# Performance work log

Hardware: AMD Instinct MI355X
Metric: run time of the kernel (lower is better)

The kernel has to match this reference:

```python
import jax, jax.numpy as jnp
import numpy as np
from jax import lax

B, L, W, C, H = 2, 64, 64, 128, 4
DH = C // H  # 32
SCALE = 32 ** -0.5  # dim_head ** -0.5
BN_EPS = 1e-3  # keras BatchNormalization default epsilon


def _sep_conv(x, dwk, dwb, g, b, mu, var, pwk, pwb):
    # Depthwise 3x3 conv, 'same' padding (NHWC, kernel HWIO with groups=C)
    y = lax.conv_general_dilated(
        x, dwk, window_strides=(1, 1), padding='SAME',
        dimension_numbers=('NHWC', 'HWIO', 'NHWC'),
        feature_group_count=x.shape[-1]) + dwb
    # BatchNorm (inference mode: moving statistics)
    y = g * (y - mu) * lax.rsqrt(var + BN_EPS) + b
    # Pointwise 1x1 conv
    return jnp.einsum('blwc,cf->blwf', y, pwk) + pwb


def setup_inputs() -> dict:
    key = jax.random.key(0)
    ks = jax.random.split(key, 32)
    d = {'x': jax.random.normal(ks[0], (B, L * W, C), dtype=jnp.float32)}
    i = 1
    for p in ('q', 'k', 'v'):
        d[p + '_dwk'] = jax.random.normal(ks[i], (3, 3, 1, C), jnp.float32) * 0.1; i += 1
        d[p + '_dwb'] = jax.random.normal(ks[i], (C,), jnp.float32) * 0.05; i += 1
        d[p + '_g'] = jnp.ones((C,), jnp.float32) + jax.random.normal(ks[i], (C,), jnp.float32) * 0.05; i += 1
        d[p + '_b'] = jax.random.normal(ks[i], (C,), jnp.float32) * 0.05; i += 1
        d[p + '_mu'] = jax.random.normal(ks[i], (C,), jnp.float32) * 0.05; i += 1
        d[p + '_var'] = jnp.abs(jax.random.normal(ks[i], (C,), jnp.float32) * 0.1) + 0.9; i += 1
        d[p + '_pwk'] = jax.random.normal(ks[i], (C, C), jnp.float32) * (C ** -0.5); i += 1
        d[p + '_pwb'] = jax.random.normal(ks[i], (C,), jnp.float32) * 0.05; i += 1
    d['out_w'] = jax.random.normal(ks[i], (C, C), jnp.float32) * (C ** -0.5); i += 1
    d['out_b'] = jax.random.normal(ks[i], (C,), jnp.float32) * 0.05
    return d


def reference(x,
              q_dwk, q_dwb, q_g, q_b, q_mu, q_var, q_pwk, q_pwb,
              k_dwk, k_dwb, k_g, k_b, k_mu, k_var, k_pwk, k_pwb,
              v_dwk, v_dwb, v_g, v_b, v_mu, v_var, v_pwk, v_pwb,
              out_w, out_b):
    xi = x.reshape(B, L, W, C)  # 'b (l w) c -> b l w c'
    def heads(t):  # 'b l w (h d) -> b h (l w) d'
        return t.reshape(B, L * W, H, DH).transpose(0, 2, 1, 3)
    q = heads(_sep_conv(xi, q_dwk, q_dwb, q_g, q_b, q_mu, q_var, q_pwk, q_pwb))
    k = heads(_sep_conv(xi, k_dwk, k_dwb, k_g, k_b, k_mu, k_var, k_pwk, k_pwb))
    v = heads(_sep_conv(xi, v_dwk, v_dwb, v_g, v_b, v_mu, v_var, v_pwk, v_pwb))
    dots = jnp.einsum('bhid,bhjd->bhij', q, k) * SCALE
    attn = jax.nn.softmax(dots, axis=-1)
    out = jnp.einsum('bhij,bhjd->bhid', attn, v)
    out = out.transpose(0, 2, 1, 3).reshape(B, L * W, C)  # 'b h c d -> b c (h d)'
    return out @ out_w + out_b  # to_out Dense (dropout is identity at inference)
```

## Files before the change

### kernel.cpp

```cpp
#include <hip/hip_runtime.h>
#include <hip/hip_bf16.h>

#define NN 4096
#define CC 128

typedef __bf16 bf16x8_t __attribute__((ext_vector_type(8)));
typedef __bf16 bf16x4_t __attribute__((ext_vector_type(4)));
typedef float f32x4 __attribute__((ext_vector_type(4)));

static constexpr float SCALE = 0.17677669529663687f;
static constexpr float BN_EPS = 1e-3f;

struct PrecompArgs {
    const float *g[3], *b[3], *mu[3], *var[3], *dwb[3], *pwk[3], *pwb[3];
    float *Wp[3], *bias[3];
};

__global__ void precomp_kernel(PrecompArgs A) {
    int q = blockIdx.x;
    int f = threadIdx.x;
    const float* pwk = A.pwk[q];
    float* Wp = A.Wp[q];
    float bias = A.pwb[q][f];
    for (int c = 0; c < 128; ++c) {
        float rs = rsqrtf(A.var[q][c] + BN_EPS);
        float s = A.g[q][c] * rs;
        float w = pwk[c * 128 + f];
        Wp[c * 128 + f] = s * w;
        bias += (s * (A.dwb[q][c] - A.mu[q][c]) + A.b[q][c]) * w;
    }
    A.bias[q][f] = bias;
}

struct ConvArgs {
    const float* x;
    const float* dwk[3];
    const float* Wp[3];
    const float* bias[3];
    __bf16* out[3];
};

__global__ __launch_bounds__(256) void conv_kernel(ConvArgs A) {
    int qkv  = blockIdx.x >> 8;
    int tile = blockIdx.x & 255;
    int b    = tile >> 7;
    int t32  = tile & 127;
    int n0   = t32 * 32;
    int l    = n0 >> 6;
    int w0   = n0 & 63;
    int tid  = threadIdx.x;

    __shared__ float dwl[32][128];

    const float* dwk = A.dwk[qkv];
    {
        int c  = tid & 127;
        int ph = tid >> 7;
        float kd[9];
#pragma unroll
        for (int t = 0; t < 9; ++t) kd[t] = dwk[t * 128 + c];
        float acc[16];
#pragma unroll
        for (int j = 0; j < 16; ++j) acc[j] = 0.f;
        int wbase = w0 + ph * 16;
        const float* xb = A.x + (size_t)b * NN * CC + c;
#pragma unroll
        for (int dl = 0; dl < 3; ++dl) {
            int ll = l + dl - 1;
            if (ll < 0 || ll >= 64) continue;
#pragma unroll
            for (int wx = 0; wx < 18; ++wx) {
                int ww = wbase + wx - 1;
                if (ww < 0 || ww >= 64) continue;
                float xv = xb[(ll * 64 + ww) * 128];
                if (wx < 16)               acc[wx]     += xv * kd[dl * 3 + 0];
                if (wx >= 1 && wx < 17)    acc[wx - 1] += xv * kd[dl * 3 + 1];
                if (wx >= 2)               acc[wx - 2] += xv * kd[dl * 3 + 2];
            }
        }
#pragma unroll
        for (int j = 0; j < 16; ++j) dwl[ph * 16 + j][c] = acc[j];
    }
    __syncthreads();
    {
        int fg = tid & 31;
        int pg = tid >> 5;
        const float* Wp = A.Wp[qkv];
        float a[4][4];
#pragma unroll
        for (int i = 0; i < 4; ++i)
#pragma unroll
            for (int j = 0; j < 4; ++j) a[i][j] = 0.f;
        for (int c = 0; c < 128; ++c) {
            f32x4 wv = *(const f32x4*)&Wp[c * 128 + fg * 4];
#pragma unroll
            for (int i = 0; i < 4; ++i) {
                float d = dwl[pg * 4 + i][c];
                a[i][0] += d * wv[0];
                a[i][1] += d * wv[1];
                a[i][2] += d * wv[2];
                a[i][3] += d * wv[3];
            }
        }
        f32x4 bs = *(const f32x4*)&A.bias[qkv][fg * 4];
        int f0 = fg * 4;
        int h  = f0 >> 5;
        int dh0 = f0 & 31;
        __bf16* dst = A.out[qkv] + ((size_t)(b * 4 + h) * NN) * 32 + dh0;
#pragma unroll
        for (int i = 0; i < 4; ++i) {
            int n = n0 + pg * 4 + i;
            bf16x4_t v;
            v[0] = (__bf16)(a[i][0] + bs[0]);
            v[1] = (__bf16)(a[i][1] + bs[1]);
            v[2] = (__bf16)(a[i][2] + bs[2]);
            v[3] = (__bf16)(a[i][3] + bs[3]);
            *(bf16x4_t*)(dst + (size_t)n * 32) = v;
        }
    }
}

__global__ __launch_bounds__(512, 1) void attn_kernel(
        const __bf16* __restrict__ qg, const __bf16* __restrict__ kg,
        const __bf16* __restrict__ vg, float* __restrict__ Og) {
    int bid = blockIdx.x;
    int bh  = bid >> 5;
    int qt  = bid & 31;
    int b   = bh >> 2, h = bh & 3;
    int tid = threadIdx.x;
    int wv  = tid >> 6;
    int lane = tid & 63;
    int lg  = lane >> 4;
    int lr  = lane & 15;

    __shared__ __bf16 Kl[64][40];
    __shared__ __bf16 Vt[32][88];
    __shared__ __bf16 Pl[8][16][88];

    const __bf16* qrow = qg + ((size_t)bh * NN + qt * 128 + wv * 16 + lr) * 32 + lg * 8;
    bf16x8_t Qf = *(const bf16x8_t*)qrow;
    const __bf16* Kbh = kg + (size_t)bh * NN * 32;
    const __bf16* Vbh = vg + (size_t)bh * NN * 32;

    f32x4 acc0 = {0.f, 0.f, 0.f, 0.f};
    f32x4 acc1 = {0.f, 0.f, 0.f, 0.f};
    f32x4 zero4 = {0.f, 0.f, 0.f, 0.f};
    float mr[4], ls[4];
#pragma unroll
    for (int r = 0; r < 4; ++r) { mr[r] = -1e30f; ls[r] = 0.f; }

    int srow = tid >> 3;
    int sc4  = (tid & 7) * 4;

    for (int t = 0; t < 64; ++t) {
        int k0 = t * 64;
        uint2 kkv = *(const uint2*)(Kbh + (size_t)(k0 + srow) * 32 + sc4);
        *(uint2*)&Kl[srow][sc4] = kkv;
        uint2 vvv = *(const uint2*)(Vbh + (size_t)(k0 + srow) * 32 + sc4);
        const __bf16* vp = (const __bf16*)&vvv;
#pragma unroll
        for (int j = 0; j < 4; ++j) Vt[sc4 + j][srow] = vp[j];
        __syncthreads();

        f32x4 s[4];
#pragma unroll
        for (int kb = 0; kb < 4; ++kb) {
            bf16x8_t Kf = *(const bf16x8_t*)&Kl[lr + kb * 16][lg * 8];
            s[kb] = __builtin_amdgcn_mfma_f32_16x16x32_bf16(Qf, Kf, zero4, 0, 0, 0);
        }
        float pr[4][4];
#pragma unroll
        for (int r = 0; r < 4; ++r) {
            float m = fmaxf(fmaxf(s[0][r], s[1][r]), fmaxf(s[2][r], s[3][r])) * SCALE;
            m = fmaxf(m, __shfl_xor(m, 1));
            m = fmaxf(m, __shfl_xor(m, 2));
            m = fmaxf(m, __shfl_xor(m, 4));
            m = fmaxf(m, __shfl_xor(m, 8));
            float mnew = fmaxf(mr[r], m);
            float alpha = __expf(mr[r] - mnew);
            mr[r] = mnew;
            float rsum = 0.f;
#pragma unroll
            for (int kb = 0; kb < 4; ++kb) {
                float p = __expf(s[kb][r] * SCALE - mnew);
                pr[kb][r] = p;
                rsum += p;
            }
            rsum += __shfl_xor(rsum, 1);
            rsum += __shfl_xor(rsum, 2);
            rsum += __shfl_xor(rsum, 4);
            rsum += __shfl_xor(rsum, 8);
            ls[r] = ls[r] * alpha + rsum;
            acc0[r] *= alpha;
            acc1[r] *= alpha;
        }
#pragma unroll
        for (int kb = 0; kb < 4; ++kb)
#pragma unroll
            for (int r = 0; r < 4; ++r)
                Pl[wv][lg * 4 + r][lr + kb * 16] = (__bf16)pr[kb][r];
        __syncthreads();
#pragma unroll
        for (int ks = 0; ks < 2; ++ks) {
            bf16x8_t Pf = *(const bf16x8_t*)&Pl[wv][lr][ks * 32 + lg * 8];
            bf16x8_t V0 = *(const bf16x8_t*)&Vt[lr][ks * 32 + lg * 8];
            bf16x8_t V1 = *(const bf16x8_t*)&Vt[lr + 16][ks * 32 + lg * 8];
            acc0 = __builtin_amdgcn_mfma_f32_16x16x32_bf16(Pf, V0, acc0, 0, 0, 0);
            acc1 = __builtin_amdgcn_mfma_f32_16x16x32_bf16(Pf, V1, acc1, 0, 0, 0);
        }
        __syncthreads();
    }
    int nrow = qt * 128 + wv * 16 + lg * 4;
    float* ob = Og + (size_t)b * NN * 128 + (size_t)h * 32;
#pragma unroll
    for (int r = 0; r < 4; ++r) {
        float inv = 1.f / ls[r];
        ob[(size_t)(nrow + r) * 128 + lr]      = acc0[r] * inv;
        ob[(size_t)(nrow + r) * 128 + lr + 16] = acc1[r] * inv;
    }
}

__global__ __launch_bounds__(256) void outproj_kernel(
        const float* __restrict__ Og, const float* __restrict__ ow,
        const float* __restrict__ obias, float* __restrict__ out) {
    int tile = blockIdx.x;
    int b = tile >> 7, t32 = tile & 127;
    int n0 = t32 * 32;
    int tid = threadIdx.x;
    __shared__ float Ol[32][128];
#pragma unroll
    for (int r2 = 0; r2 < 16; ++r2) {
        int idx = r2 * 256 + tid;
        int p = idx >> 7, c = idx & 127;
        Ol[p][c] = Og[((size_t)b * NN + n0 + p) * 128 + c];
    }
    __syncthreads();
    int fg = tid & 31, pg = tid >> 5;
    float a[4][4];
#pragma unroll
    for (int i = 0; i < 4; ++i)
#pragma unroll
        for (int j = 0; j < 4; ++j) a[i][j] = 0.f;
    for (int c = 0; c < 128; ++c) {
        f32x4 wv4 = *(const f32x4*)&ow[c * 128 + fg * 4];
#pragma unroll
        for (int i = 0; i < 4; ++i) {
            float d = Ol[pg * 4 + i][c];
            a[i][0] += d * wv4[0];
            a[i][1] += d * wv4[1];
            a[i][2] += d * wv4[2];
            a[i][3] += d * wv4[3];
        }
    }
    f32x4 bs = *(const f32x4*)&obias[fg * 4];
#pragma unroll
    for (int i = 0; i < 4; ++i) {
        int n = n0 + pg * 4 + i;
        f32x4 v;
        v[0] = a[i][0] + bs[0];
        v[1] = a[i][1] + bs[1];
        v[2] = a[i][2] + bs[2];
        v[3] = a[i][3] + bs[3];
        *(f32x4*)(out + ((size_t)b * NN + n) * 128 + fg * 4) = v;
    }
}

extern "C" void kernel_launch(void* const* d_in, const int* in_sizes, int n_in,
                              void* d_out, int out_size, void* d_ws, size_t ws_size,
                              hipStream_t stream) {
    const float* x = (const float*)d_in[0];
    char* ws = (char*)d_ws;

    float* Wp[3];
    float* biasp[3];
    __bf16* qkvp[3];
    for (int i = 0; i < 3; ++i) {
        Wp[i]    = (float*)(ws + (size_t)i * 65536);
        biasp[i] = (float*)(ws + 196608 + (size_t)i * 512);
        qkvp[i]  = (__bf16*)(ws + 262144 + (size_t)i * 2097152);
    }
    float* O = (float*)(ws + 262144 + 3 * (size_t)2097152);

    PrecompArgs pa;
    ConvArgs ca;
    ca.x = x;
    for (int i = 0; i < 3; ++i) {
        int base = 1 + 8 * i;
        ca.dwk[i] = (const float*)d_in[base + 0];
        pa.dwb[i] = (const float*)d_in[base + 1];
        pa.g[i]   = (const float*)d_in[base + 2];
        pa.b[i]   = (const float*)d_in[base + 3];
        pa.mu[i]  = (const float*)d_in[base + 4];
        pa.var[i] = (const float*)d_in[base + 5];
        pa.pwk[i] = (const float*)d_in[base + 6];
        pa.pwb[i] = (const float*)d_in[base + 7];
        pa.Wp[i] = Wp[i];
        pa.bias[i] = biasp[i];
        ca.Wp[i] = Wp[i];
        ca.bias[i] = biasp[i];
        ca.out[i] = qkvp[i];
    }

    hipLaunchKernelGGL(precomp_kernel, dim3(3), dim3(128), 0, stream, pa);
    hipLaunchKernelGGL(conv_kernel, dim3(768), dim3(256), 0, stream, ca);
    hipLaunchKernelGGL(attn_kernel, dim3(256), dim3(512), 0, stream,
                       qkvp[0], qkvp[1], qkvp[2], O);
    hipLaunchKernelGGL(outproj_kernel, dim3(256), dim3(256), 0, stream,
                       O, (const float*)d_in[25], (const float*)d_in[26],
                       (float*)d_out);
}
```

Measured before the change: 341.0 us.

## Restructure attention kernel: transposed S, register-resident P, double-buffered K/V, folded scale

Computes S transposed (K as the A operand) so each lane holds one query's 16 scores. P stays in registers as the MFMA A operand, which removes the P shared-memory round trip and one barrier per tile. K/V tiles are double-buffered with the next tile's global loads issued before compute, and the launch switches to 512 blocks of 256 threads with two blocks per CU. The softmax scale and log2e are folded into the Q projection weights in precomp so exp2f can be used without a per-element multiply. The cost is extra cross-lane shuffles to broadcast alpha and the row sum, plus more LDS for the double buffers.

```diff
diff --git a/kernel.cpp b/kernel.cpp
--- a/kernel.cpp
+++ b/kernel.cpp
@@ -9,6 +9,7 @@
 typedef float f32x4 __attribute__((ext_vector_type(4)));
 
 static constexpr float SCALE = 0.17677669529663687f;
+static constexpr float LOG2E = 1.4426950408889634f;
 static constexpr float BN_EPS = 1e-3f;
 
 struct PrecompArgs {
@@ -16,20 +17,28 @@
     float *Wp[3], *bias[3];
 };
 
-__global__ void precomp_kernel(PrecompArgs A) {
+__global__ __launch_bounds__(128) void precomp_kernel(PrecompArgs A) {
     int q = blockIdx.x;
     int f = threadIdx.x;
+    __shared__ float sS[128], sB[128];
+    {
+        int c = f;
+        float rs = rsqrtf(A.var[q][c] + BN_EPS);
+        float s = A.g[q][c] * rs;
+        sS[c] = s;
+        sB[c] = s * (A.dwb[q][c] - A.mu[q][c]) + A.b[q][c];
+    }
+    __syncthreads();
+    float qs = (q == 0) ? SCALE * LOG2E : 1.0f;
     const float* pwk = A.pwk[q];
     float* Wp = A.Wp[q];
     float bias = A.pwb[q][f];
     for (int c = 0; c < 128; ++c) {
-        float rs = rsqrtf(A.var[q][c] + BN_EPS);
-        float s = A.g[q][c] * rs;
         float w = pwk[c * 128 + f];
-        Wp[c * 128 + f] = s * w;
-        bias += (s * (A.dwb[q][c] - A.mu[q][c]) + A.b[q][c]) * w;
-    }
-    A.bias[q][f] = bias;
+        Wp[c * 128 + f] = qs * sS[c] * w;
+        bias += sB[c] * w;
+    }
+    A.bias[q][f] = qs * bias;
 }
 
 struct ConvArgs {
@@ -120,12 +129,12 @@
     }
 }
 
-__global__ __launch_bounds__(512, 1) void attn_kernel(
+__global__ __launch_bounds__(256, 2) void attn_kernel(
         const __bf16* __restrict__ qg, const __bf16* __restrict__ kg,
         const __bf16* __restrict__ vg, float* __restrict__ Og) {
     int bid = blockIdx.x;
-    int bh  = bid >> 5;
-    int qt  = bid & 31;
+    int bh  = bid & 7;
+    int qt  = bid >> 3;
     int b   = bh >> 2, h = bh & 3;
     int tid = threadIdx.x;
     int wv  = tid >> 6;
@@ -133,88 +142,112 @@
     int lg  = lane >> 4;
     int lr  = lane & 15;
 
-    __shared__ __bf16 Kl[64][40];
-    __shared__ __bf16 Vt[32][88];
-    __shared__ __bf16 Pl[8][16][88];
-
-    const __bf16* qrow = qg + ((size_t)bh * NN + qt * 128 + wv * 16 + lr) * 32 + lg * 8;
-    bf16x8_t Qf = *(const bf16x8_t*)qrow;
+    __shared__ __bf16 Kl[2][64][40];
+    __shared__ __bf16 Vt[2][32][68];
+
     const __bf16* Kbh = kg + (size_t)bh * NN * 32;
     const __bf16* Vbh = vg + (size_t)bh * NN * 32;
+
+    int qrow0 = qt * 64 + wv * 16;
+    bf16x8_t Qf = *(const bf16x8_t*)(qg + ((size_t)bh * NN + qrow0 + lr) * 32 + lg * 8);
 
     f32x4 acc0 = {0.f, 0.f, 0.f, 0.f};
     f32x4 acc1 = {0.f, 0.f, 0.f, 0.f};
     f32x4 zero4 = {0.f, 0.f, 0.f, 0.f};
-    float mr[4], ls[4];
-#pragma unroll
-    for (int r = 0; r < 4; ++r) { mr[r] = -1e30f; ls[r] = 0.f; }
-
-    int srow = tid >> 3;
-    int sc4  = (tid & 7) * 4;
-
+    float mr = -1e30f, lsum = 0.f;
+
+    int skey = tid >> 2;
+    int sdh8 = (tid & 3) * 8;
+
+    {
+        uint4 kk = *(const uint4*)(Kbh + (size_t)skey * 32 + sdh8);
+        uint4 vv = *(const uint4*)(Vbh + (size_t)skey * 32 + sdh8);
+        *(uint4*)&Kl[0][skey][sdh8] = kk;
+        const __bf16* vp = (const __bf16*)&vv;
+#pragma unroll
+        for (int j = 0; j < 8; ++j) Vt[0][sdh8 + j][skey] = vp[j];
+    }
+    __syncthreads();
+
+    uint4 kk, vv;
     for (int t = 0; t < 64; ++t) {
-        int k0 = t * 64;
-        uint2 kkv = *(const uint2*)(Kbh + (size_t)(k0 + srow) * 32 + sc4);
-        *(uint2*)&Kl[srow][sc4] = kkv;
-        uint2 vvv = *(const uint2*)(Vbh + (size_t)(k0 + srow) * 32 + sc4);
-        const __bf16* vp = (const __bf16*)&vvv;
-#pragma unroll
-        for (int j = 0; j < 4; ++j) Vt[sc4 + j][srow] = vp[j];
+        int cur = t & 1;
+        if (t < 63) {
+            int k0n = (t + 1) * 64;
+            kk = *(const uint4*)(Kbh + (size_t)(k0n + skey) * 32 + sdh8);
+            vv = *(const uint4*)(Vbh + (size_t)(k0n + skey) * 32 + sdh8);
+        }
+        f32x4 s[4];
+#pragma unroll
+        for (int kb = 0; kb < 4; ++kb) {
+            bf16x8_t Kf = *(const bf16x8_t*)&Kl[cur][kb * 16 + lr][lg * 8];
+            s[kb] = __builtin_amdgcn_mfma_f32_16x16x32_bf16(Kf, Qf, zero4, 0, 0, 0);
+        }
+        float tm = -1e30f;
+#pragma unroll
+        for (int kb = 0; kb < 4; ++kb)
+#pragma unroll
+            for (int r = 0; r < 4; ++r) tm = fmaxf(tm, s[kb][r]);
+        tm = fmaxf(tm, __shfl_xor(tm, 16));
+        tm = fmaxf(tm, __shfl_xor(tm, 32));
+        float mnew = fmaxf(mr, tm);
+        float alpha = exp2f(mr - mnew);
+        mr = mnew;
+        float p[16];
+        float rsum = 0.f;
+#pragma unroll
+        for (int kb = 0; kb < 4; ++kb)
+#pragma unroll
+            for (int r = 0; r < 4; ++r) {
+                float pv = exp2f(s[kb][r] - mnew);
+                p[kb * 4 + r] = pv;
+                rsum += pv;
+            }
+        rsum += __shfl_xor(rsum, 16);
+        rsum += __shfl_xor(rsum, 32);
+        lsum = lsum * alpha + rsum;
+#pragma unroll
+        for (int r = 0; r < 4; ++r) {
+            float ao = __shfl(alpha, lg * 4 + r);
+            acc0[r] *= ao;
+            acc1[r] *= ao;
+        }
+        bf16x8_t PA0, PA1;
+#pragma unroll
+        for (int j = 0; j < 8; ++j) {
+            PA0[j] = (__bf16)p[j];
+            PA1[j] = (__bf16)p[8 + j];
+        }
+#pragma unroll
+        for (int m = 0; m < 2; ++m) {
+            bf16x8_t Pf = (m == 0) ? PA0 : PA1;
+            bf16x4_t a0 = *(const bf16x4_t*)&Vt[cur][lr][32 * m + 4 * lg];
+            bf16x4_t a1 = *(const bf16x4_t*)&Vt[cur][lr][32 * m + 16 + 4 * lg];
+            bf16x8_t B0;
+#pragma unroll
+            for (int j = 0; j < 4; ++j) { B0[j] = a0[j]; B0[4 + j] = a1[j]; }
+            acc0 = __builtin_amdgcn_mfma_f32_16x16x32_bf16(Pf, B0, acc0, 0, 0, 0);
+            bf16x4_t c0 = *(const bf16x4_t*)&Vt[cur][lr + 16][32 * m + 4 * lg];
+            bf16x4_t c1 = *(const bf16x4_t*)&Vt[cur][lr + 16][32 * m + 16 + 4 * lg];
+            bf16x8_t B1;
+#pragma unroll
+            for (int j = 0; j < 4; ++j) { B1[j] = c0[j]; B1[4 + j] = c1[j]; }
+            acc1 = __builtin_amdgcn_mfma_f32_16x16x32_bf16(Pf, B1, acc1, 0, 0, 0);
+        }
+        if (t < 63) {
+            *(uint4*)&Kl[cur ^ 1][skey][sdh8] = kk;
+            const __bf16* vp = (const __bf16*)&vv;
+#pragma unroll
+            for (int j = 0; j < 8; ++j) Vt[cur ^ 1][sdh8 + j][skey] = vp[j];
+        }
         __syncthreads();
-
-        f32x4 s[4];
-#pragma unroll
-        for (int kb = 0; kb < 4; ++kb) {
-            bf16x8_t Kf = *(const bf16x8_t*)&Kl[lr + kb * 16][lg * 8];
-            s[kb] = __builtin_amdgcn_mfma_f32_16x16x32_bf16(Qf, Kf, zero4, 0, 0, 0);
-        }
-        float pr[4][4];
-#pragma unroll
-        for (int r = 0; r < 4; ++r) {
-            float m = fmaxf(fmaxf(s[0][r], s[1][r]), fmaxf(s[2][r], s[3][r])) * SCALE;
-            m = fmaxf(m, __shfl_xor(m, 1));
-            m = fmaxf(m, __shfl_xor(m, 2));
-            m = fmaxf(m, __shfl_xor(m, 4));
-            m = fmaxf(m, __shfl_xor(m, 8));
-            float mnew = fmaxf(mr[r], m);
-            float alpha = __expf(mr[r] - mnew);
-            mr[r] = mnew;
-            float rsum = 0.f;
-#pragma unroll
-            for (int kb = 0; kb < 4; ++kb) {
-                float p = __expf(s[kb][r] * SCALE - mnew);
-                pr[kb][r] = p;
-                rsum += p;
-            }
-            rsum += __shfl_xor(rsum, 1);
-            rsum += __shfl_xor(rsum, 2);
-            rsum += __shfl_xor(rsum, 4);
-            rsum += __shfl_xor(rsum, 8);
-            ls[r] = ls[r] * alpha + rsum;
-            acc0[r] *= alpha;
-            acc1[r] *= alpha;
-        }
-#pragma unroll
-        for (int kb = 0; kb < 4; ++kb)
-#pragma unroll
-            for (int r = 0; r < 4; ++r)
-                Pl[wv][lg * 4 + r][lr + kb * 16] = (__bf16)pr[kb][r];
-        __syncthreads();
-#pragma unroll
-        for (int ks = 0; ks < 2; ++ks) {
-            bf16x8_t Pf = *(const bf16x8_t*)&Pl[wv][lr][ks * 32 + lg * 8];
-            bf16x8_t V0 = *(const bf16x8_t*)&Vt[lr][ks * 32 + lg * 8];
-            bf16x8_t V1 = *(const bf16x8_t*)&Vt[lr + 16][ks * 32 + lg * 8];
-            acc0 = __builtin_amdgcn_mfma_f32_16x16x32_bf16(Pf, V0, acc0, 0, 0, 0);
-            acc1 = __builtin_amdgcn_mfma_f32_16x16x32_bf16(Pf, V1, acc1, 0, 0, 0);
-        }
-        __syncthreads();
-    }
-    int nrow = qt * 128 + wv * 16 + lg * 4;
+    }
+
     float* ob = Og + (size_t)b * NN * 128 + (size_t)h * 32;
+    int nrow = qrow0 + lg * 4;
 #pragma unroll
     for (int r = 0; r < 4; ++r) {
-        float inv = 1.f / ls[r];
+        float inv = 1.f / __shfl(lsum, lg * 4 + r);
         ob[(size_t)(nrow + r) * 128 + lr]      = acc0[r] * inv;
         ob[(size_t)(nrow + r) * 128 + lr + 16] = acc1[r] * inv;
     }
@@ -303,7 +336,7 @@
 
     hipLaunchKernelGGL(precomp_kernel, dim3(3), dim3(128), 0, stream, pa);
     hipLaunchKernelGGL(conv_kernel, dim3(768), dim3(256), 0, stream, ca);
-    hipLaunchKernelGGL(attn_kernel, dim3(256), dim3(512), 0, stream,
+    hipLaunchKernelGGL(attn_kernel, dim3(512), dim3(256), 0, stream,
                        qkvp[0], qkvp[1], qkvp[2], O);
     hipLaunchKernelGGL(outproj_kernel, dim3(256), dim3(256), 0, stream,
                        O, (const float*)d_in[25], (const float*)d_in[26],
```

Result: faster. 293.8 us (-13.8%).
